# Kernel optimization log

Hardware: AMD Instinct MI355X
Metric: run time of the kernel (lower is better)

The kernel has to match this reference:

```python
import jax, jax.numpy as jnp
import numpy as np

NEG_INF = -1e9

def _build_tables():
    # LC0-style 73-plane encoding per from-square: planes 0..55 queen moves
    # (8 directions x 7 distances), 56..63 knight moves. to_sq[from, plane]
    # is the to-square index; valid marks on-board targets.
    to_sq = np.zeros((64, 64), np.int32)
    valid = np.zeros((64, 64), bool)
    dirs = [(1, 0), (1, 1), (0, 1), (-1, 1), (-1, 0), (-1, -1), (0, -1), (1, -1)]
    knights = [(2, 1), (1, 2), (-1, 2), (-2, 1), (-2, -1), (-1, -2), (1, -2), (2, -1)]
    for sq in range(64):
        r, c = divmod(sq, 8)
        for d, (dr, dc) in enumerate(dirs):
            for dist in range(1, 8):
                p = d * 7 + (dist - 1)
                nr, nc = r + dr * dist, c + dc * dist
                if 0 <= nr < 8 and 0 <= nc < 8:
                    to_sq[sq, p] = nr * 8 + nc
                    valid[sq, p] = True
        for i, (dr, dc) in enumerate(knights):
            nr, nc = r + dr, c + dc
            if 0 <= nr < 8 and 0 <= nc < 8:
                to_sq[sq, 56 + i] = nr * 8 + nc
                valid[sq, 56 + i] = True
    promo_from = (np.arange(64) // 8) == 6  # rank 7 pawns (0-indexed rank 6)
    return to_sq, valid, promo_from

TO_SQ_NP, VALID_NP, PROMO_FROM_NP = _build_tables()
TO_SQ = jnp.asarray(TO_SQ_NP)            # (64, 64) int32
TO_VALID = jnp.asarray(VALID_NP)         # (64, 64) bool
PROMO_FROM = jnp.asarray(PROMO_FROM_NP)  # (64,) bool

EMBED_DIM = 1024
POLICY_DIM = 128
SCALE = POLICY_DIM ** (-0.5)


def setup_inputs() -> dict:
    key = jax.random.key(0)
    ks = jax.random.split(key, 4)
    B = 1024
    std = 1.0 / np.sqrt(EMBED_DIM)
    x = jax.random.normal(ks[0], (B, 64, EMBED_DIM), dtype=jnp.float32)
    Wq = jax.random.normal(ks[1], (EMBED_DIM, POLICY_DIM), dtype=jnp.float32) * std
    Wk = jax.random.normal(ks[2], (EMBED_DIM, POLICY_DIM), dtype=jnp.float32) * std
    Wu = jax.random.normal(ks[3], (EMBED_DIM, 9), dtype=jnp.float32) * std
    bq = jnp.zeros((POLICY_DIM,), jnp.float32)
    bk = jnp.zeros((POLICY_DIM,), jnp.float32)
    bu = jnp.zeros((9,), jnp.float32)
    return {"x": x, "Wq": Wq, "bq": bq, "Wk": Wk, "bk": bk, "Wu": Wu, "bu": bu}


def reference(x, Wq, bq, Wk, bk, Wu, bu):
    b = x.shape[0]
    q = jnp.einsum('bsd,dp->bsp', x, Wq) + bq            # (B, 64, P)
    k = jnp.einsum('bsd,dp->bsp', x, Wk) + bk            # (B, 64, P)
    logits_ft = jnp.einsum('bfp,btp->bft', q, k) * SCALE  # (B, 64, 64)
    # gather to-square logits into plane order per from-square
    idx = jnp.broadcast_to(TO_SQ[None].astype(jnp.int32), (b, 64, 64))
    logits_64 = jnp.take_along_axis(logits_ft, idx, axis=-1)  # (B, 64, 64)
    logits_64 = jnp.where(TO_VALID[None], logits_64, jnp.float32(NEG_INF))
    up = jnp.einsum('bsd,dn->bsn', x, Wu) + bu            # (B, 64, 9)
    up = jnp.where(PROMO_FROM[None, :, None], up, jnp.float32(NEG_INF))
    logits = jnp.concatenate([logits_64, up], axis=-1)    # (B, 64, 73)
    return logits.reshape(b, 64 * 73)
```

## Files before the change

### kernel.cpp

```cpp
#include <hip/hip_runtime.h>

#define NEG_INF (-1e9f)
#define SCALE_F 0.08838834764831845f

typedef __attribute__((ext_vector_type(8))) short short8;
typedef __attribute__((ext_vector_type(4))) float float4v;

__device__ __constant__ int cDR[8] = {1,1,0,-1,-1,-1,0,1};
__device__ __constant__ int cDC[8] = {0,1,1,1,0,-1,-1,-1};
__device__ __constant__ int cKR[8] = {2,1,-1,-2,-2,-1,1,2};
__device__ __constant__ int cKC[8] = {1,2,2,1,-1,-2,-2,-1};

__device__ __forceinline__ ushort f2bf(float f) {
  union { float f; unsigned u; } a; a.f = f;
  unsigned u = a.u;
  return (ushort)((u + 0x7FFFu + ((u >> 16) & 1u)) >> 16);
}

__device__ __forceinline__ void glds16(const void* g, void* l) {
  __builtin_amdgcn_global_load_lds(
      (const __attribute__((address_space(1))) unsigned int*)g,
      (__attribute__((address_space(3))) unsigned int*)l, 16, 0, 0);
}

__device__ __forceinline__ short8 pack8(float4 a, float4 b) {
  union { short8 v; unsigned u[4]; } o;
  unsigned a0 = __float_as_uint(a.x), a1 = __float_as_uint(a.y);
  unsigned a2 = __float_as_uint(a.z), a3 = __float_as_uint(a.w);
  unsigned b0 = __float_as_uint(b.x), b1 = __float_as_uint(b.y);
  unsigned b2 = __float_as_uint(b.z), b3 = __float_as_uint(b.w);
  o.u[0] = (a1 & 0xFFFF0000u) | (a0 >> 16);
  o.u[1] = (a3 & 0xFFFF0000u) | (a2 >> 16);
  o.u[2] = (b1 & 0xFFFF0000u) | (b0 >> 16);
  o.u[3] = (b3 & 0xFFFF0000u) | (b2 >> 16);
  return o.v;
}

__global__ void wconv_kernel(const float* __restrict__ Wq,
                             const float* __restrict__ Wk,
                             const float* __restrict__ Wu,
                             ushort* __restrict__ Wsw) {
  int row = blockIdx.x;
  for (int k = threadIdx.x; k < 1024; k += 256) {
    float v;
    if (row < 128)      v = Wq[k * 128 + row];
    else if (row < 256) v = Wk[k * 128 + (row - 128)];
    else if (row < 265) v = Wu[k * 9 + (row - 256)];
    else                v = 0.f;
    int kc = k >> 6, kin = k & 63, seg = kin >> 3, j = kin & 7;
    int sseg = seg ^ (row & 7);
    Wsw[(size_t)kc * 18432 + row * 64 + sseg * 8 + j] = f2bf(v);
  }
}

__global__ __launch_bounds__(256, 3)
void apol_main(const float* __restrict__ x,
               const float* __restrict__ bq,
               const float* __restrict__ bk,
               const float* __restrict__ bu,
               const ushort* __restrict__ Wsw,
               float* __restrict__ out) {
  __shared__ __align__(16) char smem[53248];
  char*   xsB = smem;
  char*   wtB = smem + 16384;
  ushort* qs  = (ushort*)smem;
  ushort* ks  = (ushort*)(smem + 16896);
  float*  Sl  = (float*)smem;

  const int tid = threadIdx.x;
  const int w = tid >> 6, lane = tid & 63;
  const int l15 = lane & 15, qd = lane >> 4;
  const char* xb = (const char*)(x + (size_t)blockIdx.x * 65536);
  const char* WsB = (const char*)Wsw;

  int xsrc[4], xlds[4];
  #pragma unroll
  for (int c = 0; c < 4; ++c) {
    int g = (c * 4 + w) * 64 + lane;
    int row = g >> 4, sg = g & 15;
    xsrc[c] = row * 4096 + ((sg ^ (row & 7)) * 16);
    xlds[c] = (c * 4 + w) * 1024;
  }

  int aaddr[4][2][2];
  #pragma unroll
  for (int mt = 0; mt < 4; ++mt) {
    int row = mt * 16 + l15;
    #pragma unroll
    for (int kk = 0; kk < 2; ++kk)
      #pragma unroll
      for (int h = 0; h < 2; ++h)
        aaddr[mt][kk][h] = row * 256 + (((kk * 8 + qd * 2 + h) ^ (row & 7)) * 16);
  }
  int baddr[4][2], uaddr[2];
  #pragma unroll
  for (int nt = 0; nt < 4; ++nt) {
    int row = w * 64 + nt * 16 + l15;
    #pragma unroll
    for (int kk = 0; kk < 2; ++kk)
      baddr[nt][kk] = row * 128 + (((kk * 4 + qd) ^ (l15 & 7)) * 16);
  }
  #pragma unroll
  for (int kk = 0; kk < 2; ++kk)
    uaddr[kk] = (256 + l15) * 128 + (((kk * 4 + qd) ^ (l15 & 7)) * 16);

  float4v acc[4][4];
  #pragma unroll
  for (int i = 0; i < 4; ++i)
    #pragma unroll
    for (int j = 0; j < 4; ++j)
      acc[i][j] = (float4v){0.f, 0.f, 0.f, 0.f};
  float4v aup = (float4v){0.f, 0.f, 0.f, 0.f};

  #pragma unroll 1
  for (int kc = 0; kc < 16; ++kc) {
    #pragma unroll
    for (int c = 0; c < 4; ++c)
      glds16(xb + kc * 256 + xsrc[c], xsB + xlds[c]);
    const char* wsrc = WsB + (size_t)kc * 36864 + (size_t)lane * 16;
    #pragma unroll
    for (int c = 0; c < 9; ++c)
      glds16(wsrc + (c * 4 + w) * 1024, wtB + (c * 4 + w) * 1024);
    __syncthreads();

    #pragma unroll
    for (int kk = 0; kk < 2; ++kk) {
      short8 af[4];
      #pragma unroll
      for (int mt = 0; mt < 4; ++mt) {
        float4 g0 = *(const float4*)(xsB + aaddr[mt][kk][0]);
        float4 g1 = *(const float4*)(xsB + aaddr[mt][kk][1]);
        af[mt] = pack8(g0, g1);
      }
      short8 bf[4];
      #pragma unroll
      for (int nt = 0; nt < 4; ++nt)
        bf[nt] = *(const short8*)(wtB + baddr[nt][kk]);
      #pragma unroll
      for (int mt = 0; mt < 4; ++mt)
        #pragma unroll
        for (int nt = 0; nt < 4; ++nt)
          acc[mt][nt] = __builtin_amdgcn_mfma_f32_16x16x32_bf16(
              af[mt], bf[nt], acc[mt][nt], 0, 0, 0);
      if (w == 3) {
        short8 ub = *(const short8*)(wtB + uaddr[kk]);
        aup = __builtin_amdgcn_mfma_f32_16x16x32_bf16(af[3], ub, aup, 0, 0, 0);
      }
    }
    __syncthreads();
  }

  float* outb = out + (size_t)blockIdx.x * 4672;

  if (w == 3 && qd < 2 && l15 < 9) {
    float bias = bu[l15];
    #pragma unroll
    for (int r = 0; r < 4; ++r) {
      int f = 48 + qd * 4 + r;
      outb[f * 73 + 64 + l15] = aup[r] + bias;
    }
  }

  #pragma unroll
  for (int nt = 0; nt < 4; ++nt) {
    int C = w * 64 + nt * 16 + l15;
    bool isq = (C < 128);
    int p = isq ? C : (C - 128);
    float bias = isq ? bq[p] : bk[p];
    ushort* dstb = isq ? qs : ks;
    #pragma unroll
    for (int mt = 0; mt < 4; ++mt)
      #pragma unroll
      for (int r = 0; r < 4; ++r) {
        int row = mt * 16 + qd * 4 + r;
        float v = acc[mt][nt][r] + bias;
        if (isq) v *= SCALE_F;
        dstb[row * 132 + p] = f2bf(v);
      }
  }
  __syncthreads();

  float4v acc2[4];
  #pragma unroll
  for (int nt = 0; nt < 4; ++nt) acc2[nt] = (float4v){0.f, 0.f, 0.f, 0.f};
  #pragma unroll
  for (int kp = 0; kp < 4; ++kp) {
    int kb = kp * 32 + qd * 8;
    short8 a2 = *(const short8*)((const char*)&qs[(w * 16 + l15) * 132 + kb]);
    #pragma unroll
    for (int nt = 0; nt < 4; ++nt) {
      short8 b2 = *(const short8*)((const char*)&ks[(nt * 16 + l15) * 132 + kb]);
      acc2[nt] = __builtin_amdgcn_mfma_f32_16x16x32_bf16(a2, b2, acc2[nt], 0, 0, 0);
    }
  }
  __syncthreads();
  #pragma unroll
  for (int nt = 0; nt < 4; ++nt)
    #pragma unroll
    for (int r = 0; r < 4; ++r)
      Sl[(w * 16 + qd * 4 + r) * 65 + nt * 16 + l15] = acc2[nt][r];
  __syncthreads();

  for (int idx = tid; idx < 4672; idx += 256) {
    int f = idx / 73;
    int j = idx - f * 73;
    float val;
    if (j < 64) {
      int rr = f >> 3, cc = f & 7;
      int nr, nc;
      if (j < 56) {
        int d = j / 7;
        int dist = j - d * 7 + 1;
        nr = rr + cDR[d] * dist;
        nc = cc + cDC[d] * dist;
      } else {
        nr = rr + cKR[j - 56];
        nc = cc + cKC[j - 56];
      }
      val = (nr >= 0 && nr < 8 && nc >= 0 && nc < 8) ? Sl[f * 65 + nr * 8 + nc]
                                                     : NEG_INF;
    } else {
      if (f >= 48 && f < 56) continue;
      val = NEG_INF;
    }
    outb[idx] = val;
  }
}

extern "C" void kernel_launch(void* const* d_in, const int* in_sizes, int n_in,
                              void* d_out, int out_size, void* d_ws, size_t ws_size,
                              hipStream_t stream) {
  const float* x  = (const float*)d_in[0];
  const float* Wq = (const float*)d_in[1];
  const float* bq = (const float*)d_in[2];
  const float* Wk = (const float*)d_in[3];
  const float* bk = (const float*)d_in[4];
  const float* Wu = (const float*)d_in[5];
  const float* bu = (const float*)d_in[6];
  float* out = (float*)d_out;
  ushort* Wsw = (ushort*)d_ws;

  const int B = in_sizes[0] / 65536;

  wconv_kernel<<<288, 256, 0, stream>>>(Wq, Wk, Wu, Wsw);
  apol_main<<<B, 256, 0, stream>>>(x, bq, bk, bu, Wsw, out);
}
```

Baseline: 405.7 us.

## Process two batch elements per block to reuse weight tiles

Each block now handles two boards (128 rows) instead of one, doubling the x tile staged in LDS and the MFMA accumulator set. Each staged weight chunk then feeds twice as many rows, cutting the weight load traffic into LDS per unit of work. In exchange, register and LDS use grow, occupancy drops from 3 to 2 blocks per CU, and the grid halves.

```diff
diff --git a/kernel.cpp b/kernel.cpp
--- a/kernel.cpp
+++ b/kernel.cpp
@@ -53,45 +53,43 @@
   }
 }
 
-__global__ __launch_bounds__(256, 3)
+__global__ __launch_bounds__(256, 2)
 void apol_main(const float* __restrict__ x,
                const float* __restrict__ bq,
                const float* __restrict__ bk,
                const float* __restrict__ bu,
                const ushort* __restrict__ Wsw,
                float* __restrict__ out) {
-  __shared__ __align__(16) char smem[53248];
+  __shared__ __align__(16) char smem[69632];
   char*   xsB = smem;
-  char*   wtB = smem + 16384;
+  char*   wtB = smem + 32768;
   ushort* qs  = (ushort*)smem;
-  ushort* ks  = (ushort*)(smem + 16896);
+  ushort* ks  = (ushort*)(smem + 33792);
   float*  Sl  = (float*)smem;
 
   const int tid = threadIdx.x;
   const int w = tid >> 6, lane = tid & 63;
   const int l15 = lane & 15, qd = lane >> 4;
-  const char* xb = (const char*)(x + (size_t)blockIdx.x * 65536);
+  const char* xb = (const char*)(x + (size_t)blockIdx.x * 131072);
   const char* WsB = (const char*)Wsw;
 
-  int xsrc[4], xlds[4];
-  #pragma unroll
-  for (int c = 0; c < 4; ++c) {
+  int xsrc[8];
+  #pragma unroll
+  for (int c = 0; c < 8; ++c) {
     int g = (c * 4 + w) * 64 + lane;
-    int row = g >> 4, sg = g & 15;
-    xsrc[c] = row * 4096 + ((sg ^ (row & 7)) * 16);
-    xlds[c] = (c * 4 + w) * 1024;
-  }
-
-  int aaddr[4][2][2];
-  #pragma unroll
-  for (int mt = 0; mt < 4; ++mt) {
-    int row = mt * 16 + l15;
-    #pragma unroll
-    for (int kk = 0; kk < 2; ++kk)
-      #pragma unroll
-      for (int h = 0; h < 2; ++h)
-        aaddr[mt][kk][h] = row * 256 + (((kk * 8 + qd * 2 + h) ^ (row & 7)) * 16);
-  }
+    int e = g >> 10, gg = g & 1023;
+    int row = gg >> 4, sg = gg & 15;
+    xsrc[c] = e * 262144 + row * 4096 + ((sg ^ (row & 7)) * 16);
+  }
+
+  int xoff[2][2];
+  #pragma unroll
+  for (int kk = 0; kk < 2; ++kk)
+    #pragma unroll
+    for (int h = 0; h < 2; ++h)
+      xoff[kk][h] = (((kk * 8 + qd * 2 + h) ^ (l15 & 7)) * 16);
+  const int arow = l15 * 256;
+
   int baddr[4][2], uaddr[2];
   #pragma unroll
   for (int nt = 0; nt < 4; ++nt) {
@@ -104,19 +102,21 @@
   for (int kk = 0; kk < 2; ++kk)
     uaddr[kk] = (256 + l15) * 128 + (((kk * 4 + qd) ^ (l15 & 7)) * 16);
 
-  float4v acc[4][4];
-  #pragma unroll
-  for (int i = 0; i < 4; ++i)
+  float4v acc[8][4];
+  #pragma unroll
+  for (int i = 0; i < 8; ++i)
     #pragma unroll
     for (int j = 0; j < 4; ++j)
       acc[i][j] = (float4v){0.f, 0.f, 0.f, 0.f};
-  float4v aup = (float4v){0.f, 0.f, 0.f, 0.f};
+  float4v aup[2];
+  aup[0] = (float4v){0.f, 0.f, 0.f, 0.f};
+  aup[1] = (float4v){0.f, 0.f, 0.f, 0.f};
 
   #pragma unroll 1
   for (int kc = 0; kc < 16; ++kc) {
     #pragma unroll
-    for (int c = 0; c < 4; ++c)
-      glds16(xb + kc * 256 + xsrc[c], xsB + xlds[c]);
+    for (int c = 0; c < 8; ++c)
+      glds16(xb + kc * 256 + xsrc[c], xsB + (c * 4 + w) * 1024);
     const char* wsrc = WsB + (size_t)kc * 36864 + (size_t)lane * 16;
     #pragma unroll
     for (int c = 0; c < 9; ++c)
@@ -125,39 +125,39 @@
 
     #pragma unroll
     for (int kk = 0; kk < 2; ++kk) {
-      short8 af[4];
-      #pragma unroll
-      for (int mt = 0; mt < 4; ++mt) {
-        float4 g0 = *(const float4*)(xsB + aaddr[mt][kk][0]);
-        float4 g1 = *(const float4*)(xsB + aaddr[mt][kk][1]);
-        af[mt] = pack8(g0, g1);
-      }
       short8 bf[4];
       #pragma unroll
       for (int nt = 0; nt < 4; ++nt)
         bf[nt] = *(const short8*)(wtB + baddr[nt][kk]);
-      #pragma unroll
-      for (int mt = 0; mt < 4; ++mt)
+      short8 ub;
+      if (w == 3) ub = *(const short8*)(wtB + uaddr[kk]);
+      #pragma unroll
+      for (int mt = 0; mt < 8; ++mt) {
+        float4 g0 = *(const float4*)(xsB + mt * 4096 + arow + xoff[kk][0]);
+        float4 g1 = *(const float4*)(xsB + mt * 4096 + arow + xoff[kk][1]);
+        short8 af = pack8(g0, g1);
         #pragma unroll
         for (int nt = 0; nt < 4; ++nt)
           acc[mt][nt] = __builtin_amdgcn_mfma_f32_16x16x32_bf16(
-              af[mt], bf[nt], acc[mt][nt], 0, 0, 0);
-      if (w == 3) {
-        short8 ub = *(const short8*)(wtB + uaddr[kk]);
-        aup = __builtin_amdgcn_mfma_f32_16x16x32_bf16(af[3], ub, aup, 0, 0, 0);
+              af, bf[nt], acc[mt][nt], 0, 0, 0);
+        if (w == 3 && (mt & 3) == 3)
+          aup[mt >> 2] = __builtin_amdgcn_mfma_f32_16x16x32_bf16(
+              af, ub, aup[mt >> 2], 0, 0, 0);
       }
     }
     __syncthreads();
   }
-
-  float* outb = out + (size_t)blockIdx.x * 4672;
 
   if (w == 3 && qd < 2 && l15 < 9) {
     float bias = bu[l15];
     #pragma unroll
-    for (int r = 0; r < 4; ++r) {
-      int f = 48 + qd * 4 + r;
-      outb[f * 73 + 64 + l15] = aup[r] + bias;
+    for (int e = 0; e < 2; ++e) {
+      float* oe = out + (size_t)(blockIdx.x * 2 + e) * 4672;
+      #pragma unroll
+      for (int r = 0; r < 4; ++r) {
+        int f = 48 + qd * 4 + r;
+        oe[f * 73 + 64 + l15] = aup[e][r] + bias;
+      }
     }
   }
 
@@ -169,61 +169,73 @@
     float bias = isq ? bq[p] : bk[p];
     ushort* dstb = isq ? qs : ks;
     #pragma unroll
-    for (int mt = 0; mt < 4; ++mt)
+    for (int mt = 0; mt < 8; ++mt)
       #pragma unroll
       for (int r = 0; r < 4; ++r) {
         int row = mt * 16 + qd * 4 + r;
+        int e = row >> 6, sr = row & 63;
         float v = acc[mt][nt][r] + bias;
         if (isq) v *= SCALE_F;
-        dstb[row * 132 + p] = f2bf(v);
+        dstb[e * 8448 + sr * 132 + p] = f2bf(v);
       }
   }
   __syncthreads();
 
-  float4v acc2[4];
-  #pragma unroll
-  for (int nt = 0; nt < 4; ++nt) acc2[nt] = (float4v){0.f, 0.f, 0.f, 0.f};
-  #pragma unroll
-  for (int kp = 0; kp < 4; ++kp) {
-    int kb = kp * 32 + qd * 8;
-    short8 a2 = *(const short8*)((const char*)&qs[(w * 16 + l15) * 132 + kb]);
-    #pragma unroll
-    for (int nt = 0; nt < 4; ++nt) {
-      short8 b2 = *(const short8*)((const char*)&ks[(nt * 16 + l15) * 132 + kb]);
-      acc2[nt] = __builtin_amdgcn_mfma_f32_16x16x32_bf16(a2, b2, acc2[nt], 0, 0, 0);
-    }
-  }
+  float4v acc2[2][4];
+  #pragma unroll
+  for (int e = 0; e < 2; ++e)
+    #pragma unroll
+    for (int nt = 0; nt < 4; ++nt) acc2[e][nt] = (float4v){0.f, 0.f, 0.f, 0.f};
+  #pragma unroll
+  for (int e = 0; e < 2; ++e)
+    #pragma unroll
+    for (int kp = 0; kp < 4; ++kp) {
+      int kb = kp * 32 + qd * 8;
+      short8 a2 = *(const short8*)((const char*)&qs[e * 8448 + (w * 16 + l15) * 132 + kb]);
+      #pragma unroll
+      for (int nt = 0; nt < 4; ++nt) {
+        short8 b2 = *(const short8*)((const char*)&ks[e * 8448 + (nt * 16 + l15) * 132 + kb]);
+        acc2[e][nt] = __builtin_amdgcn_mfma_f32_16x16x32_bf16(a2, b2, acc2[e][nt], 0, 0, 0);
+      }
+    }
   __syncthreads();
   #pragma unroll
-  for (int nt = 0; nt < 4; ++nt)
-    #pragma unroll
-    for (int r = 0; r < 4; ++r)
-      Sl[(w * 16 + qd * 4 + r) * 65 + nt * 16 + l15] = acc2[nt][r];
+  for (int e = 0; e < 2; ++e)
+    #pragma unroll
+    for (int nt = 0; nt < 4; ++nt)
+      #pragma unroll
+      for (int r = 0; r < 4; ++r)
+        Sl[e * 4160 + (w * 16 + qd * 4 + r) * 65 + nt * 16 + l15] = acc2[e][nt][r];
   __syncthreads();
 
-  for (int idx = tid; idx < 4672; idx += 256) {
-    int f = idx / 73;
-    int j = idx - f * 73;
-    float val;
-    if (j < 64) {
-      int rr = f >> 3, cc = f & 7;
-      int nr, nc;
-      if (j < 56) {
-        int d = j / 7;
-        int dist = j - d * 7 + 1;
-        nr = rr + cDR[d] * dist;
-        nc = cc + cDC[d] * dist;
+  #pragma unroll 1
+  for (int e = 0; e < 2; ++e) {
+    float* oe = out + (size_t)(blockIdx.x * 2 + e) * 4672;
+    const float* Se = Sl + e * 4160;
+    for (int idx = tid; idx < 4672; idx += 256) {
+      int f = idx / 73;
+      int j = idx - f * 73;
+      float val;
+      if (j < 64) {
+        int rr = f >> 3, cc = f & 7;
+        int nr, nc;
+        if (j < 56) {
+          int d = j / 7;
+          int dist = j - d * 7 + 1;
+          nr = rr + cDR[d] * dist;
+          nc = cc + cDC[d] * dist;
+        } else {
+          nr = rr + cKR[j - 56];
+          nc = cc + cKC[j - 56];
+        }
+        val = (nr >= 0 && nr < 8 && nc >= 0 && nc < 8) ? Se[f * 65 + nr * 8 + nc]
+                                                       : NEG_INF;
       } else {
-        nr = rr + cKR[j - 56];
-        nc = cc + cKC[j - 56];
-      }
-      val = (nr >= 0 && nr < 8 && nc >= 0 && nc < 8) ? Sl[f * 65 + nr * 8 + nc]
-                                                     : NEG_INF;
-    } else {
-      if (f >= 48 && f < 56) continue;
-      val = NEG_INF;
-    }
-    outb[idx] = val;
+        if (f >= 48 && f < 56) continue;
+        val = NEG_INF;
+      }
+      oe[idx] = val;
+    }
   }
 }
 
@@ -243,5 +255,5 @@
   const int B = in_sizes[0] / 65536;
 
   wconv_kernel<<<288, 256, 0, stream>>>(Wq, Wk, Wu, Wsw);
-  apol_main<<<B, 256, 0, stream>>>(x, bq, bk, bu, Wsw, out);
-}
+  apol_main<<<B / 2, 256, 0, stream>>>(x, bq, bk, bu, Wsw, out);
+}
```

Measured after the change: 417.7 us. 1.03x slower.

## Double-buffer bf16 x tiles in LDS and read weights directly from global

Applied to the files above, without the earlier changes.

The x tile is now converted to bf16 once when it is staged into a double-buffered LDS tile, with register prefetch of the next k-chunk overlapping the MFMA work, instead of raw fp32 being staged via global_load_lds and repacked per use. Weight fragments are loaded straight from global (L2-resident) in an unswizzled layout rather than staged through LDS. This cuts the LDS footprint, which may allow more resident blocks, and halves the barriers per chunk. In exchange the MFMAs now depend on global-memory weight loads in the inner loop, adding latency.

```diff
diff --git a/kernel.cpp b/kernel.cpp
--- a/kernel.cpp
+++ b/kernel.cpp
@@ -15,12 +15,6 @@
   union { float f; unsigned u; } a; a.f = f;
   unsigned u = a.u;
   return (ushort)((u + 0x7FFFu + ((u >> 16) & 1u)) >> 16);
-}
-
-__device__ __forceinline__ void glds16(const void* g, void* l) {
-  __builtin_amdgcn_global_load_lds(
-      (const __attribute__((address_space(1))) unsigned int*)g,
-      (__attribute__((address_space(3))) unsigned int*)l, 16, 0, 0);
 }
 
 __device__ __forceinline__ short8 pack8(float4 a, float4 b) {
@@ -47,9 +41,8 @@
     else if (row < 256) v = Wk[k * 128 + (row - 128)];
     else if (row < 265) v = Wu[k * 9 + (row - 256)];
     else                v = 0.f;
-    int kc = k >> 6, kin = k & 63, seg = kin >> 3, j = kin & 7;
-    int sseg = seg ^ (row & 7);
-    Wsw[(size_t)kc * 18432 + row * 64 + sseg * 8 + j] = f2bf(v);
+    int kc = k >> 6, kin = k & 63;
+    Wsw[(size_t)kc * 18432 + row * 64 + kin] = f2bf(v);
   }
 }
 
@@ -60,9 +53,9 @@
                const float* __restrict__ bu,
                const ushort* __restrict__ Wsw,
                float* __restrict__ out) {
-  __shared__ __align__(16) char smem[53248];
-  char*   xsB = smem;
-  char*   wtB = smem + 16384;
+  __shared__ __align__(16) char smem[33792];
+  char*   xs0 = smem;
+  char*   xs1 = smem + 8192;
   ushort* qs  = (ushort*)smem;
   ushort* ks  = (ushort*)(smem + 16896);
   float*  Sl  = (float*)smem;
@@ -73,36 +66,20 @@
   const char* xb = (const char*)(x + (size_t)blockIdx.x * 65536);
   const char* WsB = (const char*)Wsw;
 
-  int xsrc[4], xlds[4];
-  #pragma unroll
-  for (int c = 0; c < 4; ++c) {
-    int g = (c * 4 + w) * 64 + lane;
-    int row = g >> 4, sg = g & 15;
-    xsrc[c] = row * 4096 + ((sg ^ (row & 7)) * 16);
-    xlds[c] = (c * 4 + w) * 1024;
-  }
-
-  int aaddr[4][2][2];
-  #pragma unroll
-  for (int mt = 0; mt < 4; ++mt) {
-    int row = mt * 16 + l15;
-    #pragma unroll
-    for (int kk = 0; kk < 2; ++kk)
-      #pragma unroll
-      for (int h = 0; h < 2; ++h)
-        aaddr[mt][kk][h] = row * 256 + (((kk * 8 + qd * 2 + h) ^ (row & 7)) * 16);
-  }
-  int baddr[4][2], uaddr[2];
-  #pragma unroll
-  for (int nt = 0; nt < 4; ++nt) {
-    int row = w * 64 + nt * 16 + l15;
-    #pragma unroll
-    for (int kk = 0; kk < 2; ++kk)
-      baddr[nt][kk] = row * 128 + (((kk * 4 + qd) ^ (l15 & 7)) * 16);
-  }
+  const int srow = w * 16 + (lane >> 2);
+  const int scol4 = lane & 3;
+  const char* xsrc = xb + srow * 4096 + scol4 * 64;
+  const int wr0 = srow * 128 + (((scol4 * 2 + 0) ^ (srow & 7)) * 16);
+  const int wr1 = srow * 128 + (((scol4 * 2 + 1) ^ (srow & 7)) * 16);
+
+  const int arow = l15 * 128;
+  int aoff[2];
   #pragma unroll
   for (int kk = 0; kk < 2; ++kk)
-    uaddr[kk] = (256 + l15) * 128 + (((kk * 4 + qd) ^ (l15 & 7)) * 16);
+    aoff[kk] = (((kk * 4 + qd) ^ (l15 & 7)) * 16);
+
+  const int wvo = (w * 64 + l15) * 128 + qd * 16;
+  const int uvo = (256 + l15) * 128 + qd * 16;
 
   float4v acc[4][4];
   #pragma unroll
@@ -112,40 +89,52 @@
       acc[i][j] = (float4v){0.f, 0.f, 0.f, 0.f};
   float4v aup = (float4v){0.f, 0.f, 0.f, 0.f};
 
+  {
+    float4 g0 = *(const float4*)(xsrc);
+    float4 g1 = *(const float4*)(xsrc + 16);
+    float4 g2 = *(const float4*)(xsrc + 32);
+    float4 g3 = *(const float4*)(xsrc + 48);
+    *(short8*)(xs0 + wr0) = pack8(g0, g1);
+    *(short8*)(xs0 + wr1) = pack8(g2, g3);
+  }
+  __syncthreads();
+
   #pragma unroll 1
   for (int kc = 0; kc < 16; ++kc) {
-    #pragma unroll
-    for (int c = 0; c < 4; ++c)
-      glds16(xb + kc * 256 + xsrc[c], xsB + xlds[c]);
-    const char* wsrc = WsB + (size_t)kc * 36864 + (size_t)lane * 16;
-    #pragma unroll
-    for (int c = 0; c < 9; ++c)
-      glds16(wsrc + (c * 4 + w) * 1024, wtB + (c * 4 + w) * 1024);
-    __syncthreads();
-
+    const char* xcur = (kc & 1) ? xs1 : xs0;
+    char* xnxt = (kc & 1) ? xs0 : xs1;
+    float4 g0, g1, g2, g3;
+    const bool pf = (kc < 15);
+    if (pf) {
+      const char* s = xsrc + (kc + 1) * 256;
+      g0 = *(const float4*)(s);
+      g1 = *(const float4*)(s + 16);
+      g2 = *(const float4*)(s + 32);
+      g3 = *(const float4*)(s + 48);
+    }
+    const char* wp = WsB + (size_t)kc * 36864;
     #pragma unroll
     for (int kk = 0; kk < 2; ++kk) {
-      short8 af[4];
-      #pragma unroll
-      for (int mt = 0; mt < 4; ++mt) {
-        float4 g0 = *(const float4*)(xsB + aaddr[mt][kk][0]);
-        float4 g1 = *(const float4*)(xsB + aaddr[mt][kk][1]);
-        af[mt] = pack8(g0, g1);
-      }
       short8 bf[4];
       #pragma unroll
       for (int nt = 0; nt < 4; ++nt)
-        bf[nt] = *(const short8*)(wtB + baddr[nt][kk]);
+        bf[nt] = *(const short8*)(wp + wvo + nt * 2048 + kk * 64);
+      short8 ub;
+      if (w == 3) ub = *(const short8*)(wp + uvo + kk * 64);
       #pragma unroll
-      for (int mt = 0; mt < 4; ++mt)
+      for (int mt = 0; mt < 4; ++mt) {
+        short8 af = *(const short8*)(xcur + mt * 2048 + arow + aoff[kk]);
         #pragma unroll
         for (int nt = 0; nt < 4; ++nt)
           acc[mt][nt] = __builtin_amdgcn_mfma_f32_16x16x32_bf16(
-              af[mt], bf[nt], acc[mt][nt], 0, 0, 0);
-      if (w == 3) {
-        short8 ub = *(const short8*)(wtB + uaddr[kk]);
-        aup = __builtin_amdgcn_mfma_f32_16x16x32_bf16(af[3], ub, aup, 0, 0, 0);
+              af, bf[nt], acc[mt][nt], 0, 0, 0);
+        if (w == 3 && mt == 3)
+          aup = __builtin_amdgcn_mfma_f32_16x16x32_bf16(af, ub, aup, 0, 0, 0);
       }
+    }
+    if (pf) {
+      *(short8*)(xnxt + wr0) = pack8(g0, g1);
+      *(short8*)(xnxt + wr1) = pack8(g2, g3);
     }
     __syncthreads();
   }
```

Result: slower. 470.5 us (+16.0%).
